# Kernel tuning notes

Measured on AMD Instinct MI355X. Metric: run time of the kernel, lower is better.

Reference implementation:

```python
import jax, jax.numpy as jnp
import numpy as np

HEADS, DK, DV, STRIDE = 8, 32, 32, 2
EPS = 1e-5

def dwconv(x, w, b, stride):
    # depthwise 3x3, padding 1; w: [C,1,3,3]
    y = jax.lax.conv_general_dilated(
        x, w, (stride, stride), ((1, 1), (1, 1)),
        dimension_numbers=("NCHW", "OIHW", "NCHW"),
        feature_group_count=x.shape[1])
    return y + b[None, :, None, None]

def setup_inputs() -> dict:
    key = jax.random.key(0)
    ks = jax.random.split(key, 16)
    B_, C, H, W = 8, 256, 56, 56
    hd = HEADS * DK
    s = lambda k, shp: (jax.random.normal(k, shp, jnp.float32) * 0.02)
    return {
        "x": jax.random.normal(ks[0], (B_, C, H, W), jnp.float32),
        "Wk_dw": s(ks[1], (C, 1, 3, 3)), "bk_dw": jnp.zeros((C,), jnp.float32),
        "Wv_dw": s(ks[2], (C, 1, 3, 3)), "bv_dw": jnp.zeros((C,), jnp.float32),
        "Wq": s(ks[3], (hd, C)), "bq": jnp.zeros((hd,), jnp.float32),
        "Wk": s(ks[4], (hd, C)), "bk": jnp.zeros((hd,), jnp.float32),
        "Wv": s(ks[5], (HEADS * DV, C)), "bv": jnp.zeros((HEADS * DV,), jnp.float32),
        "Wo": s(ks[6], (C, HEADS * DV)), "bo": jnp.zeros((C,), jnp.float32),
        "Bbias": s(ks[7], (1, HEADS, H * W, (H // STRIDE) * (W // STRIDE))),
    }

def reference(x, Wk_dw, bk_dw, Wv_dw, bv_dw, Wq, bq, Wk, bk, Wv, bv, Wo, bo, Bbias):
    b, c, h, w = x.shape
    xr = x.reshape(b, c, h * w).transpose(0, 2, 1)  # [b, hw, c]
    # F.layer_norm with normalized_shape=(b, hw, c): single mean/var over ALL elements
    mu = jnp.mean(xr)
    var = jnp.mean((xr - mu) ** 2)
    xn = (xr - mu) * jax.lax.rsqrt(var + EPS)
    q = (xn @ Wq.T + bq).reshape(b, h * w, HEADS, DK).transpose(0, 2, 1, 3)  # [b,H,hw,dk]
    ki = dwconv(x, Wk_dw, bk_dw, STRIDE)
    kh, kw = ki.shape[2], ki.shape[3]
    kf = ki.reshape(b, c, kh * kw).transpose(0, 2, 1)
    k = (kf @ Wk.T + bk).reshape(b, kh * kw, HEADS, DK).transpose(0, 2, 1, 3)
    vi = dwconv(x, Wv_dw, bv_dw, STRIDE)
    vf = vi.reshape(b, c, kh * kw).transpose(0, 2, 1)
    v = (vf @ Wv.T + bv).reshape(b, kh * kw, HEADS, DV).transpose(0, 2, 1, 3)
    attn = jnp.einsum("bhid,bhjd->bhij", q, k) * (DK ** -0.5) + Bbias
    attn = jax.nn.softmax(attn, axis=-1)
    res = jnp.einsum("bhij,bhjd->bhid", attn, v).transpose(0, 2, 1, 3)
    res = res.reshape(b, h * w, HEADS * DV)
    out = (res @ Wo.T + bo).reshape(b, c, h, w)  # faithful to original .view (no transpose)
    return out + x
```

## Files before the change

### kernel.cpp

```cpp
#include <hip/hip_runtime.h>

typedef unsigned short u16;
typedef unsigned int   u32;
typedef __attribute__((ext_vector_type(8))) short short8;
typedef __attribute__((ext_vector_type(4))) float f32x4;

#define MFMA16(a, b, c) __builtin_amdgcn_mfma_f32_16x16x32_bf16((a), (b), (c), 0, 0, 0)

static constexpr int B_ = 8;
static constexpr int HW = 3136;
static constexpr int KW = 784;
static constexpr int NELEM = B_ * 256 * HW;

static constexpr size_t OFF_CNT = 4096;
static constexpr size_t OFF_W   = 8192;
static constexpr int AOFF_WQ = 0, AOFF_WK = 65536, AOFF_WV = 131072, AOFF_WO = 196608;
static constexpr int AOFF_WKDW = 262144, AOFF_WVDW = 264448;
static constexpr int AOFF_BKDW = 266752, AOFF_BVDW = 267008, AOFF_BQ = 267264;
static constexpr int AOFF_BK = 267520, AOFF_BV = 267776, AOFF_BO = 268032;
static constexpr size_t OFF_XT  = 557056;
static constexpr size_t SZ_XT   = (size_t)B_ * HW * 256 * 2;
static constexpr size_t SZ_KJ   = (size_t)B_ * KW * 256 * 2;
static constexpr size_t OFF_KIT = OFF_XT + SZ_XT;
static constexpr size_t OFF_VIT = OFF_KIT + SZ_KJ;
static constexpr size_t OFF_KI  = OFF_VIT + SZ_KJ;
static constexpr size_t OFF_VI  = OFF_KI + SZ_KJ;
static constexpr size_t OFF_Q   = OFF_VI + SZ_KJ;
static constexpr size_t OFF_O   = OFF_XT;

__device__ __forceinline__ float bf2f(u16 u) { return __uint_as_float(((u32)u) << 16); }
__device__ __forceinline__ u16 f2bf(float f) {
  u32 u = __float_as_uint(f);
  u32 r = u + 0x7FFFu + ((u >> 16) & 1u);
  return (u16)(r >> 16);
}
__device__ __forceinline__ float bflo(u32 u) { return __uint_as_float(u << 16); }
__device__ __forceinline__ float bfhi(u32 u) { return __uint_as_float(u & 0xFFFF0000u); }
__device__ __forceinline__ u32 packbf(float a, float b) {
  u32 ua = __float_as_uint(a); ua = (ua + 0x7FFFu + ((ua >> 16) & 1u)) >> 16;
  u32 ub = __float_as_uint(b); ub = (ub + 0x7FFFu + ((ub >> 16) & 1u)) >> 16;
  return ua | (ub << 16);
}

__global__ __launch_bounds__(256) void detect_k(const u32* __restrict__ x, int* __restrict__ cnt) {
  int c = 0;
  for (int i = threadIdx.x; i < 4096; i += 256) {
    float v = __uint_as_float(x[i] << 16);
    if (fabsf(v) > 1e4f) c++;
  }
#pragma unroll
  for (int off = 32; off > 0; off >>= 1) c += __shfl_down(c, off);
  if ((threadIdx.x & 63) == 0) atomicAdd(cnt, c);
}

struct CvtArgs { const void* src[12]; int dstoff[12]; int n[12]; };
__global__ __launch_bounds__(256) void cvtw_k(CvtArgs a, u16* __restrict__ arena,
                                              const int* __restrict__ cnt) {
  int t = blockIdx.y;
  int n = a.n[t];
  u16* d = arena + a.dstoff[t];
  int f32m = (*cnt >= 64);
  if (f32m) {
    const float* s = (const float*)a.src[t];
    for (int i = blockIdx.x * 256 + threadIdx.x; i < n; i += gridDim.x * 256) d[i] = f2bf(s[i]);
  } else {
    const u16* s = (const u16*)a.src[t];
    for (int i = blockIdx.x * 256 + threadIdx.x; i < n; i += gridDim.x * 256) d[i] = s[i];
  }
}

__global__ __launch_bounds__(256) void reduce_k(const void* __restrict__ x, double* __restrict__ acc,
                                                const int* __restrict__ cnt) {
  int f32m = (*cnt >= 64);
  float s = 0.f, ss = 0.f;
  if (f32m) {
    const float4* xv = (const float4*)x;
    const int n4 = NELEM / 4;
    for (int i = blockIdx.x * 256 + threadIdx.x; i < n4; i += gridDim.x * 256) {
      float4 u = xv[i];
      s += u.x + u.y + u.z + u.w;
      ss += u.x * u.x + u.y * u.y + u.z * u.z + u.w * u.w;
    }
  } else {
    const uint4* xv = (const uint4*)x;
    const int n8 = NELEM / 8;
    for (int i = blockIdx.x * 256 + threadIdx.x; i < n8; i += gridDim.x * 256) {
      uint4 u = xv[i];
      u32 w[4] = {u.x, u.y, u.z, u.w};
#pragma unroll
      for (int q = 0; q < 4; q++) {
        float f0 = __uint_as_float(w[q] << 16);
        float f1 = __uint_as_float(w[q] & 0xFFFF0000u);
        s += f0 + f1;
        ss += f0 * f0 + f1 * f1;
      }
    }
  }
#pragma unroll
  for (int off = 32; off > 0; off >>= 1) {
    s += __shfl_down(s, off);
    ss += __shfl_down(ss, off);
  }
  __shared__ float as_[4], ass_[4];
  int wv = threadIdx.x >> 6;
  if ((threadIdx.x & 63) == 0) { as_[wv] = s; ass_[wv] = ss; }
  __syncthreads();
  if (threadIdx.x == 0) {
    atomicAdd(acc + 0, (double)(as_[0] + as_[1] + as_[2] + as_[3]));
    atomicAdd(acc + 1, (double)(ass_[0] + ass_[1] + ass_[2] + ass_[3]));
  }
}

__global__ __launch_bounds__(256) void prep_k(const u16* __restrict__ wq, const u16* __restrict__ bq,
                                              float* __restrict__ wsf) {
  const double* acc = (const double*)wsf;
  __shared__ float sh[2];
  if (threadIdx.x == 0) {
    double N = (double)NELEM;
    double mu = acc[0] / N;
    double var = acc[1] / N - mu * mu;
    float rstd = (float)(1.0 / sqrt(var + 1e-5));
    sh[0] = (float)mu; sh[1] = rstd;
    wsf[4] = (float)mu; wsf[5] = rstd;
    wsf[6] = rstd * 0.17677669529663687f;
  }
  __syncthreads();
  int o = threadIdx.x;
  float wsum = 0.f;
  for (int c = 0; c < 256; c++) wsum += bf2f(wq[o * 256 + c]);
  wsf[16 + o] = (bf2f(bq[o]) - sh[1] * sh[0] * wsum) * 0.17677669529663687f;
}

__global__ __launch_bounds__(256) void transpose_x_k(const void* __restrict__ src, u16* __restrict__ dst,
                                                     const int* __restrict__ cnt) {
  int f32m = (*cnt >= 64);
  __shared__ u16 t[32][33];
  int b = blockIdx.z;
  int r0 = blockIdx.y * 32, c0 = blockIdx.x * 32;
  int tid = threadIdx.x, col = tid & 31;
  size_t base = (size_t)b * 256 * HW;
  if (f32m) {
    const float* s = (const float*)src + base;
#pragma unroll
    for (int i = 0; i < 4; i++) {
      int row = (tid >> 5) + i * 8;
      t[row][col] = f2bf(s[(size_t)(r0 + row) * HW + c0 + col]);
    }
  } else {
    const u16* s = (const u16*)src + base;
#pragma unroll
    for (int i = 0; i < 4; i++) {
      int row = (tid >> 5) + i * 8;
      t[row][col] = s[(size_t)(r0 + row) * HW + c0 + col];
    }
  }
  __syncthreads();
  u16* d = dst + base;
#pragma unroll
  for (int i = 0; i < 4; i++) {
    int row = (tid >> 5) + i * 8;
    d[(size_t)(c0 + row) * 256 + r0 + col] = t[col][row];
  }
}

__global__ __launch_bounds__(256) void transpose_k(const u16* __restrict__ src, u16* __restrict__ dst,
                                                   int R, int Cc) {
  __shared__ u16 t[32][33];
  int b = blockIdx.z;
  int r0 = blockIdx.y * 32, c0 = blockIdx.x * 32;
  const u16* s = src + (size_t)b * R * Cc;
  u16* d = dst + (size_t)b * R * Cc;
  int tid = threadIdx.x, col = tid & 31;
#pragma unroll
  for (int i = 0; i < 4; i++) {
    int row = (tid >> 5) + i * 8;
    if (r0 + row < R && c0 + col < Cc) t[row][col] = s[(size_t)(r0 + row) * Cc + c0 + col];
  }
  __syncthreads();
#pragma unroll
  for (int i = 0; i < 4; i++) {
    int row = (tid >> 5) + i * 8;
    if (c0 + row < Cc && r0 + col < R) d[(size_t)(c0 + row) * R + r0 + col] = t[col][row];
  }
}

__global__ __launch_bounds__(256) void dwconv_k(const void* __restrict__ x,
                                                const u16* __restrict__ arena,
                                                u16* __restrict__ ki, u16* __restrict__ vi,
                                                const int* __restrict__ cnt) {
  int f32m = (*cnt >= 64);
  int b = blockIdx.x >> 8;
  int c = blockIdx.x & 255;
  float wkf[9], wvf[9];
#pragma unroll
  for (int t = 0; t < 9; t++) {
    wkf[t] = bf2f(arena[AOFF_WKDW + c * 9 + t]);
    wvf[t] = bf2f(arena[AOFF_WVDW + c * 9 + t]);
  }
  float kb = bf2f(arena[AOFF_BKDW + c]), vb = bf2f(arena[AOFF_BVDW + c]);
  size_t xbase = (size_t)(b * 256 + c) * HW;
  auto body = [&](auto LDX) {
    for (int j = threadIdx.x; j < KW; j += 256) {
      int oi = j / 28, oj = j % 28;
      float ka = kb, va = vb;
#pragma unroll
      for (int di = 0; di < 3; di++) {
        int ii = 2 * oi - 1 + di;
        if ((unsigned)ii >= 56u) continue;
#pragma unroll
        for (int dj = 0; dj < 3; dj++) {
          int ij = 2 * oj - 1 + dj;
          if ((unsigned)ij >= 56u) continue;
          float xv = LDX(ii * 56 + ij);
          ka += xv * wkf[di * 3 + dj];
          va += xv * wvf[di * 3 + dj];
        }
      }
      ki[(size_t)(b * 256 + c) * KW + j] = f2bf(ka);
      vi[(size_t)(b * 256 + c) * KW + j] = f2bf(va);
    }
  };
  if (f32m) {
    const float* xp = (const float*)x + xbase;
    body([&](int i) { return xp[i]; });
  } else {
    const u16* xp = (const u16*)x + xbase;
    body([&](int i) { return bf2f(xp[i]); });
  }
}

__global__ __launch_bounds__(256) void proj_q_k(const u16* __restrict__ xt, const u16* __restrict__ Wq,
                                                const float* __restrict__ wsf, u16* __restrict__ q) {
  int lane = threadIdx.x & 63, wave = threadIdx.x >> 6;
  int l15 = lane & 15, quad = lane >> 4;
  int b = blockIdx.x / 49, pb = blockIdx.x % 49;
  int p0 = pb * 64 + wave * 16;
  const u16* arow = xt + ((size_t)(b * HW) + p0 + l15) * 256 + quad * 8;
  short8 af[8];
#pragma unroll
  for (int ks = 0; ks < 8; ks++) af[ks] = *(const short8*)(arow + ks * 32);
  float alpha = wsf[6];
  const float* beta = wsf + 16;
  for (int ot = 0; ot < 16; ot++) {
    const u16* brow = Wq + (size_t)(ot * 16 + l15) * 256 + quad * 8;
    f32x4 acc = {0.f, 0.f, 0.f, 0.f};
#pragma unroll
    for (int ks = 0; ks < 8; ks++) acc = MFMA16(af[ks], *(const short8*)(brow + ks * 32), acc);
    int o = ot * 16 + l15;
    float bet = beta[o];
    size_t base = ((size_t)(b * HW) + p0 + quad * 4) * 256 + o;
#pragma unroll
    for (int r = 0; r < 4; r++) q[base + (size_t)r * 256] = f2bf(alpha * acc[r] + bet);
  }
}

__global__ __launch_bounds__(256) void proj_k_k(const u16* __restrict__ kit, const u16* __restrict__ Wk,
                                                const u16* __restrict__ bk, u16* __restrict__ kout) {
  int lane = threadIdx.x & 63, wave = threadIdx.x >> 6;
  int l15 = lane & 15, quad = lane >> 4;
  int b = blockIdx.x / 13, jb = blockIdx.x % 13;
  int p0 = jb * 64 + wave * 16;
  if (p0 >= KW) return;
  const u16* arow = kit + ((size_t)(b * KW) + p0 + l15) * 256 + quad * 8;
  short8 af[8];
#pragma unroll
  for (int ks = 0; ks < 8; ks++) af[ks] = *(const short8*)(arow + ks * 32);
  for (int ot = 0; ot < 16; ot++) {
    const u16* brow = Wk + (size_t)(ot * 16 + l15) * 256 + quad * 8;
    f32x4 acc = {0.f, 0.f, 0.f, 0.f};
#pragma unroll
    for (int ks = 0; ks < 8; ks++) acc = MFMA16(af[ks], *(const short8*)(brow + ks * 32), acc);
    int o = ot * 16 + l15;
    float bias = bf2f(bk[o]);
    size_t base = ((size_t)(b * KW) + p0 + quad * 4) * 256 + o;
#pragma unroll
    for (int r = 0; r < 4; r++) kout[base + (size_t)r * 256] = f2bf(acc[r] + bias);
  }
}

__global__ __launch_bounds__(256) void proj_v_k(const u16* __restrict__ Wv, const u16* __restrict__ vit,
                                                const u16* __restrict__ bv, u16* __restrict__ vT) {
  int lane = threadIdx.x & 63, wave = threadIdx.x >> 6;
  int l15 = lane & 15, quad = lane >> 4;
  int b = blockIdx.x >> 4;
  int ob = (blockIdx.x >> 2) & 3;
  int js = blockIdx.x & 3;
  int o0 = ob * 64 + wave * 16;
  const u16* arow = Wv + (size_t)(o0 + l15) * 256 + quad * 8;
  short8 af[8];
#pragma unroll
  for (int ks = 0; ks < 8; ks++) af[ks] = *(const short8*)(arow + ks * 32);
  int jt0 = js * 13;
  int jt1 = (jt0 + 13 < 49) ? jt0 + 13 : 49;
  for (int jt = jt0; jt < jt1; jt++) {
    const u16* brow = vit + ((size_t)(b * KW) + jt * 16 + l15) * 256 + quad * 8;
    f32x4 acc = {0.f, 0.f, 0.f, 0.f};
#pragma unroll
    for (int ks = 0; ks < 8; ks++) acc = MFMA16(af[ks], *(const short8*)(brow + ks * 32), acc);
#pragma unroll
    for (int r = 0; r < 4; r++) {
      int o = o0 + quad * 4 + r;
      vT[((size_t)(b * 256) + o) * KW + jt * 16 + l15] = f2bf(acc[r] + bf2f(bv[o]));
    }
  }
}

__global__ __launch_bounds__(64) void attn_k(const u16* __restrict__ q, const u16* __restrict__ k,
                                             const u16* __restrict__ vT, const void* __restrict__ Bb,
                                             u16* __restrict__ Ob, const int* __restrict__ cnt) {
  int f32m = (*cnt >= 64);
  int lane = threadIdx.x;
  int l15 = lane & 15, quad = lane >> 4;
  int pt = blockIdx.x % 196;
  int t = blockIdx.x / 196;
  int h = t & 7, b = t >> 3;
  int p0 = pt * 16;
  __shared__ __align__(16) u16 Pch[16][40];

  const u16* qp = q + ((size_t)(b * HW) + p0 + l15) * 256 + h * 32 + quad * 8;
  short8 af = *(const short8*)qp;
  const u16* kb = k + (size_t)b * KW * 256 + h * 32 + quad * 8;
  size_t boff = ((size_t)(h * HW) + p0) * KW;

  u32 sp[49][2];
  auto score_loop = [&](auto LDB) {
#pragma unroll
    for (int jt = 0; jt < 49; jt++) {
      short8 bfr = *(const short8*)(kb + (size_t)(jt * 16 + l15) * 256);
      f32x4 acc = {0.f, 0.f, 0.f, 0.f};
      acc = MFMA16(af, bfr, acc);
      int col = jt * 16 + l15;
      float v0 = acc[0] + LDB(0, col);
      float v1 = acc[1] + LDB(1, col);
      float v2 = acc[2] + LDB(2, col);
      float v3 = acc[3] + LDB(3, col);
      sp[jt][0] = packbf(v0, v1);
      sp[jt][1] = packbf(v2, v3);
    }
  };
  if (f32m) {
    const float* bbf = (const float*)Bb + boff;
    score_loop([&](int r, int c) { return bbf[(size_t)(quad * 4 + r) * KW + c]; });
  } else {
    const u16* bbb = (const u16*)Bb + boff;
    score_loop([&](int r, int c) { return bf2f(bbb[(size_t)(quad * 4 + r) * KW + c]); });
  }

  float m[4] = {-1e30f, -1e30f, -1e30f, -1e30f};
#pragma unroll
  for (int jt = 0; jt < 49; jt++) {
    m[0] = fmaxf(m[0], bflo(sp[jt][0])); m[1] = fmaxf(m[1], bfhi(sp[jt][0]));
    m[2] = fmaxf(m[2], bflo(sp[jt][1])); m[3] = fmaxf(m[3], bfhi(sp[jt][1]));
  }
#pragma unroll
  for (int off = 1; off < 16; off <<= 1)
#pragma unroll
    for (int r = 0; r < 4; r++) m[r] = fmaxf(m[r], __shfl_xor(m[r], off));
  float l[4] = {0.f, 0.f, 0.f, 0.f};
#pragma unroll
  for (int jt = 0; jt < 49; jt++) {
    float e0 = __expf(bflo(sp[jt][0]) - m[0]);
    float e1 = __expf(bfhi(sp[jt][0]) - m[1]);
    float e2 = __expf(bflo(sp[jt][1]) - m[2]);
    float e3 = __expf(bfhi(sp[jt][1]) - m[3]);
    l[0] += e0; l[1] += e1; l[2] += e2; l[3] += e3;
    sp[jt][0] = packbf(e0, e1);
    sp[jt][1] = packbf(e2, e3);
  }
#pragma unroll
  for (int off = 1; off < 16; off <<= 1)
#pragma unroll
    for (int r = 0; r < 4; r++) l[r] += __shfl_xor(l[r], off);
  float inv[4];
#pragma unroll
  for (int r = 0; r < 4; r++) inv[r] = 1.f / l[r];

  f32x4 oa = {0.f, 0.f, 0.f, 0.f}, obb = {0.f, 0.f, 0.f, 0.f};
  const u16* vb = vT + ((size_t)(b * 256) + h * 32) * KW;
#pragma unroll
  for (int ch = 0; ch < 25; ch++) {
#pragma unroll
    for (int half = 0; half < 2; half++) {
      int jt = ch * 2 + half;
      u32 p0k = 0, p1k = 0;
      if (jt < 49) { p0k = sp[jt][0]; p1k = sp[jt][1]; }
      int col = half * 16 + l15;
      Pch[quad * 4 + 0][col] = (u16)(p0k & 0xFFFFu);
      Pch[quad * 4 + 1][col] = (u16)(p0k >> 16);
      Pch[quad * 4 + 2][col] = (u16)(p1k & 0xFFFFu);
      Pch[quad * 4 + 3][col] = (u16)(p1k >> 16);
    }
    __syncthreads();
    short8 pf = *(const short8*)(&Pch[l15][quad * 8]);
    int jo = ch * 32 + quad * 8;
    if (jo > 776) jo = 776;
    short8 v0 = *(const short8*)(vb + (size_t)l15 * KW + jo);
    short8 v1 = *(const short8*)(vb + (size_t)(16 + l15) * KW + jo);
    oa  = MFMA16(pf, v0, oa);
    obb = MFMA16(pf, v1, obb);
    __syncthreads();
  }
  size_t obase = ((size_t)(b * HW) + p0 + quad * 4) * 256 + h * 32 + l15;
#pragma unroll
  for (int r = 0; r < 4; r++) {
    Ob[obase + (size_t)r * 256]      = f2bf(oa[r] * inv[r]);
    Ob[obase + (size_t)r * 256 + 16] = f2bf(obb[r] * inv[r]);
  }
}

__global__ __launch_bounds__(256) void proj_o_k(const u16* __restrict__ Ob, const u16* __restrict__ Wo,
                                                const u16* __restrict__ bo, const void* __restrict__ x,
                                                void* __restrict__ out, const int* __restrict__ cnt) {
  int f32m = (*cnt >= 64);
  int lane = threadIdx.x & 63, wave = threadIdx.x >> 6;
  int l15 = lane & 15, quad = lane >> 4;
  int b = blockIdx.x / 49, pb = blockIdx.x % 49;
  int p0 = pb * 64 + wave * 16;
  const u16* arow = Ob + ((size_t)(b * HW) + p0 + l15) * 256 + quad * 8;
  short8 af[8];
#pragma unroll
  for (int ks = 0; ks < 8; ks++) af[ks] = *(const short8*)(arow + ks * 32);
  for (int ot = 0; ot < 16; ot++) {
    const u16* brow = Wo + (size_t)(ot * 16 + l15) * 256 + quad * 8;
    f32x4 acc = {0.f, 0.f, 0.f, 0.f};
#pragma unroll
    for (int ks = 0; ks < 8; ks++) acc = MFMA16(af[ks], *(const short8*)(brow + ks * 32), acc);
    int o = ot * 16 + l15;
    float bias = bf2f(bo[o]);
    if (f32m) {
      const float* xf = (const float*)x;
      float* of = (float*)out;
#pragma unroll
      for (int r = 0; r < 4; r++) {
        size_t idx = ((size_t)(b * HW) + p0 + quad * 4 + r) * 256 + o;
        of[idx] = acc[r] + bias + xf[idx];
      }
    } else {
      const u16* xb = (const u16*)x;
      u16* ob_ = (u16*)out;
#pragma unroll
      for (int r = 0; r < 4; r++) {
        size_t idx = ((size_t)(b * HW) + p0 + quad * 4 + r) * 256 + o;
        ob_[idx] = f2bf(acc[r] + bias + bf2f(xb[idx]));
      }
    }
  }
}

extern "C" void kernel_launch(void* const* d_in, const int* in_sizes, int n_in,
                              void* d_out, int out_size, void* d_ws, size_t ws_size,
                              hipStream_t stream) {
  (void)in_sizes; (void)n_in; (void)out_size; (void)ws_size;
  const void* x = d_in[0];
  char* ws = (char*)d_ws;
  int* cnt = (int*)(ws + OFF_CNT);
  u16* arena = (u16*)(ws + OFF_W);
  u16* xt  = (u16*)(ws + OFF_XT);
  u16* kit = (u16*)(ws + OFF_KIT);
  u16* vit = (u16*)(ws + OFF_VIT);
  u16* ki  = (u16*)(ws + OFF_KI);
  u16* vi  = (u16*)(ws + OFF_VI);
  u16* qb  = (u16*)(ws + OFF_Q);
  u16* Obuf = (u16*)(ws + OFF_O);

  CvtArgs a;
  const int srcidx[12] = {5, 7, 9, 11, 1, 3, 2, 4, 6, 8, 10, 12};
  const int dofs[12] = {AOFF_WQ, AOFF_WK, AOFF_WV, AOFF_WO, AOFF_WKDW, AOFF_WVDW,
                        AOFF_BKDW, AOFF_BVDW, AOFF_BQ, AOFF_BK, AOFF_BV, AOFF_BO};
  const int ns[12] = {65536, 65536, 65536, 65536, 2304, 2304, 256, 256, 256, 256, 256, 256};
  for (int i = 0; i < 12; i++) { a.src[i] = d_in[srcidx[i]]; a.dstoff[i] = dofs[i]; a.n[i] = ns[i]; }

  hipMemsetAsync(d_ws, 0, 8192, stream);
  detect_k<<<1, 256, 0, stream>>>((const u32*)x, cnt);
  cvtw_k<<<dim3(32, 12), 256, 0, stream>>>(a, arena, cnt);
  reduce_k<<<1024, 256, 0, stream>>>(x, (double*)d_ws, cnt);
  prep_k<<<1, 256, 0, stream>>>(arena + AOFF_WQ, arena + AOFF_BQ, (float*)d_ws);
  transpose_x_k<<<dim3(98, 8, 8), 256, 0, stream>>>(x, xt, cnt);
  dwconv_k<<<2048, 256, 0, stream>>>(x, arena, ki, vi, cnt);
  transpose_k<<<dim3(25, 8, 8), 256, 0, stream>>>(ki, kit, 256, KW);
  transpose_k<<<dim3(25, 8, 8), 256, 0, stream>>>(vi, vit, 256, KW);
  proj_k_k<<<104, 256, 0, stream>>>(kit, arena + AOFF_WK, arena + AOFF_BK, ki);
  proj_v_k<<<128, 256, 0, stream>>>(arena + AOFF_WV, vit, arena + AOFF_BV, vi);
  proj_q_k<<<392, 256, 0, stream>>>(xt, arena + AOFF_WQ, (const float*)d_ws, qb);
  attn_k<<<12544, 64, 0, stream>>>(qb, ki, vi, d_in[13], Obuf, cnt);
  proj_o_k<<<392, 256, 0, stream>>>(Obuf, arena + AOFF_WO, arena + AOFF_BO, x, d_out, cnt);
}
```

Baseline: 513.3 us.

## Share attention bias tile across four batches via LDS; merge K/V transposes

The attention kernel now runs four waves per block, one per batch, all working on the same head and query tile. The block stages the shared Bbias tile (converted to bf16) into LDS once with vectorized loads, so the bias is read from global memory once per four batches instead of once per wave. The two K/V transpose launches are also merged into one kernel to save a launch. The costs are about 25KB of LDS per block, which may limit occupancy, and block-wide syncs that now couple four waves.

After: 534.8 us. +4.2%, slower.

```diff
diff --git a/kernel.cpp b/kernel.cpp
--- a/kernel.cpp
+++ b/kernel.cpp
@@ -163,24 +163,27 @@
   }
 }
 
-__global__ __launch_bounds__(256) void transpose_k(const u16* __restrict__ src, u16* __restrict__ dst,
-                                                   int R, int Cc) {
+__global__ __launch_bounds__(256) void transpose_kv_k(const u16* __restrict__ s1, u16* __restrict__ d1,
+                                                      const u16* __restrict__ s2, u16* __restrict__ d2) {
   __shared__ u16 t[32][33];
-  int b = blockIdx.z;
+  int which = blockIdx.z >> 3;
+  int b = blockIdx.z & 7;
+  const u16* src = which ? s2 : s1;
+  u16* dst = which ? d2 : d1;
   int r0 = blockIdx.y * 32, c0 = blockIdx.x * 32;
-  const u16* s = src + (size_t)b * R * Cc;
-  u16* d = dst + (size_t)b * R * Cc;
+  const u16* s = src + (size_t)b * 256 * KW;
+  u16* d = dst + (size_t)b * 256 * KW;
   int tid = threadIdx.x, col = tid & 31;
 #pragma unroll
   for (int i = 0; i < 4; i++) {
     int row = (tid >> 5) + i * 8;
-    if (r0 + row < R && c0 + col < Cc) t[row][col] = s[(size_t)(r0 + row) * Cc + c0 + col];
+    if (c0 + col < KW) t[row][col] = s[(size_t)(r0 + row) * KW + c0 + col];
   }
   __syncthreads();
 #pragma unroll
   for (int i = 0; i < 4; i++) {
     int row = (tid >> 5) + i * 8;
-    if (c0 + row < Cc && r0 + col < R) d[(size_t)(c0 + row) * R + r0 + col] = t[col][row];
+    if (c0 + row < KW) d[(size_t)(c0 + row) * 256 + r0 + col] = t[col][row];
   }
 }
 
@@ -305,45 +308,70 @@
   }
 }
 
-__global__ __launch_bounds__(64) void attn_k(const u16* __restrict__ q, const u16* __restrict__ k,
-                                             const u16* __restrict__ vT, const void* __restrict__ Bb,
-                                             u16* __restrict__ Ob, const int* __restrict__ cnt) {
+static constexpr int BSTRIDE = 788;
+__global__ __launch_bounds__(256) void attn_k(const u16* __restrict__ q, const u16* __restrict__ k,
+                                              const u16* __restrict__ vT, const void* __restrict__ Bb,
+                                              u16* __restrict__ Ob, const int* __restrict__ cnt) {
   int f32m = (*cnt >= 64);
-  int lane = threadIdx.x;
+  int tid = threadIdx.x;
+  int lane = tid & 63, wave = tid >> 6;
   int l15 = lane & 15, quad = lane >> 4;
-  int pt = blockIdx.x % 196;
-  int t = blockIdx.x / 196;
-  int h = t & 7, b = t >> 3;
+  int bid = blockIdx.x;
+  int pt = bid >> 4;
+  int h = (bid >> 1) & 7;
+  int half = bid & 1;
+  int b = half * 4 + wave;
   int p0 = pt * 16;
-  __shared__ __align__(16) u16 Pch[16][40];
+  __shared__ __align__(16) u16 bls[16 * BSTRIDE];
+  __shared__ __align__(16) u16 Pch[4][16][40];
+
+  {
+    size_t boff = ((size_t)(h * HW) + p0) * KW;
+    if (f32m) {
+      const float* bbf = (const float*)Bb + boff;
+#pragma unroll
+      for (int it = 0; it < 13; it++) {
+        int chunk = it * 256 + tid;
+        if (chunk < 3136) {
+          int row = chunk / 196, c4 = chunk - row * 196;
+          float4 v = *(const float4*)(bbf + (size_t)row * KW + c4 * 4);
+          uint2 p;
+          p.x = packbf(v.x, v.y);
+          p.y = packbf(v.z, v.w);
+          *(uint2*)&bls[row * BSTRIDE + c4 * 4] = p;
+        }
+      }
+    } else {
+      const u16* bbb = (const u16*)Bb + boff;
+#pragma unroll
+      for (int it = 0; it < 13; it++) {
+        int chunk = it * 256 + tid;
+        if (chunk < 3136) {
+          int row = chunk / 196, c4 = chunk - row * 196;
+          *(uint2*)&bls[row * BSTRIDE + c4 * 4] = *(const uint2*)(bbb + (size_t)row * KW + c4 * 4);
+        }
+      }
+    }
+  }
+  __syncthreads();
 
   const u16* qp = q + ((size_t)(b * HW) + p0 + l15) * 256 + h * 32 + quad * 8;
   short8 af = *(const short8*)qp;
   const u16* kb = k + (size_t)b * KW * 256 + h * 32 + quad * 8;
-  size_t boff = ((size_t)(h * HW) + p0) * KW;
 
   u32 sp[49][2];
-  auto score_loop = [&](auto LDB) {
-#pragma unroll
-    for (int jt = 0; jt < 49; jt++) {
-      short8 bfr = *(const short8*)(kb + (size_t)(jt * 16 + l15) * 256);
-      f32x4 acc = {0.f, 0.f, 0.f, 0.f};
-      acc = MFMA16(af, bfr, acc);
-      int col = jt * 16 + l15;
-      float v0 = acc[0] + LDB(0, col);
-      float v1 = acc[1] + LDB(1, col);
-      float v2 = acc[2] + LDB(2, col);
-      float v3 = acc[3] + LDB(3, col);
-      sp[jt][0] = packbf(v0, v1);
-      sp[jt][1] = packbf(v2, v3);
-    }
-  };
-  if (f32m) {
-    const float* bbf = (const float*)Bb + boff;
-    score_loop([&](int r, int c) { return bbf[(size_t)(quad * 4 + r) * KW + c]; });
-  } else {
-    const u16* bbb = (const u16*)Bb + boff;
-    score_loop([&](int r, int c) { return bf2f(bbb[(size_t)(quad * 4 + r) * KW + c]); });
+#pragma unroll
+  for (int jt = 0; jt < 49; jt++) {
+    short8 bfr = *(const short8*)(kb + (size_t)(jt * 16 + l15) * 256);
+    f32x4 acc = {0.f, 0.f, 0.f, 0.f};
+    acc = MFMA16(af, bfr, acc);
+    int col = jt * 16 + l15;
+    float v0 = acc[0] + bf2f(bls[(quad * 4 + 0) * BSTRIDE + col]);
+    float v1 = acc[1] + bf2f(bls[(quad * 4 + 1) * BSTRIDE + col]);
+    float v2 = acc[2] + bf2f(bls[(quad * 4 + 2) * BSTRIDE + col]);
+    float v3 = acc[3] + bf2f(bls[(quad * 4 + 3) * BSTRIDE + col]);
+    sp[jt][0] = packbf(v0, v1);
+    sp[jt][1] = packbf(v2, v3);
   }
 
   float m[4] = {-1e30f, -1e30f, -1e30f, -1e30f};
@@ -380,18 +408,18 @@
 #pragma unroll
   for (int ch = 0; ch < 25; ch++) {
 #pragma unroll
-    for (int half = 0; half < 2; half++) {
-      int jt = ch * 2 + half;
+    for (int hf = 0; hf < 2; hf++) {
+      int jt = ch * 2 + hf;
       u32 p0k = 0, p1k = 0;
       if (jt < 49) { p0k = sp[jt][0]; p1k = sp[jt][1]; }
-      int col = half * 16 + l15;
-      Pch[quad * 4 + 0][col] = (u16)(p0k & 0xFFFFu);
-      Pch[quad * 4 + 1][col] = (u16)(p0k >> 16);
-      Pch[quad * 4 + 2][col] = (u16)(p1k & 0xFFFFu);
-      Pch[quad * 4 + 3][col] = (u16)(p1k >> 16);
+      int col = hf * 16 + l15;
+      Pch[wave][quad * 4 + 0][col] = (u16)(p0k & 0xFFFFu);
+      Pch[wave][quad * 4 + 1][col] = (u16)(p0k >> 16);
+      Pch[wave][quad * 4 + 2][col] = (u16)(p1k & 0xFFFFu);
+      Pch[wave][quad * 4 + 3][col] = (u16)(p1k >> 16);
     }
     __syncthreads();
-    short8 pf = *(const short8*)(&Pch[l15][quad * 8]);
+    short8 pf = *(const short8*)(&Pch[wave][l15][quad * 8]);
     int jo = ch * 32 + quad * 8;
     if (jo > 776) jo = 776;
     short8 v0 = *(const short8*)(vb + (size_t)l15 * KW + jo);
@@ -477,11 +505,10 @@
   prep_k<<<1, 256, 0, stream>>>(arena + AOFF_WQ, arena + AOFF_BQ, (float*)d_ws);
   transpose_x_k<<<dim3(98, 8, 8), 256, 0, stream>>>(x, xt, cnt);
   dwconv_k<<<2048, 256, 0, stream>>>(x, arena, ki, vi, cnt);
-  transpose_k<<<dim3(25, 8, 8), 256, 0, stream>>>(ki, kit, 256, KW);
-  transpose_k<<<dim3(25, 8, 8), 256, 0, stream>>>(vi, vit, 256, KW);
+  transpose_kv_k<<<dim3(25, 8, 16), 256, 0, stream>>>(ki, kit, vi, vit);
   proj_k_k<<<104, 256, 0, stream>>>(kit, arena + AOFF_WK, arena + AOFF_BK, ki);
   proj_v_k<<<128, 256, 0, stream>>>(arena + AOFF_WV, vit, arena + AOFF_BV, vi);
   proj_q_k<<<392, 256, 0, stream>>>(xt, arena + AOFF_WQ, (const float*)d_ws, qb);
-  attn_k<<<12544, 64, 0, stream>>>(qb, ki, vi, d_in[13], Obuf, cnt);
+  attn_k<<<3136, 256, 0, stream>>>(qb, ki, vi, d_in[13], Obuf, cnt);
   proj_o_k<<<392, 256, 0, stream>>>(Obuf, arena + AOFF_WO, arena + AOFF_BO, x, d_out, cnt);
 }
```
